# Kernel tuning notes

Hardware: AMD Instinct MI355X
Metric: run time of the kernel (lower is better)

## Reference

```python
import jax, jax.numpy as jnp
import numpy as np

G = 128          # graphs in batch
NPG = 2048       # nodes per graph (all graphs equal-sized; >= K so no topk padding)
N = G * NPG      # total nodes
MUT_PER_G = 2    # mutation CA atoms per graph
M = G * MUT_PER_G  # total centers (fixed for jit)
CA_ID = 1
K = 64           # module init k
BIG = jnp.float32(1e30)


def setup_inputs() -> dict:
    key = jax.random.key(0)
    k1, k2 = jax.random.split(key)
    node_position = jax.random.normal(k1, (N, 3), dtype=jnp.float32) * 10.0
    node2graph = jnp.repeat(jnp.arange(G, dtype=jnp.int32), NPG)
    local_idx = jnp.arange(N, dtype=jnp.int32) % NPG
    is_mutation = local_idx < MUT_PER_G                     # 2 mutation sites per graph
    atom_name = jax.random.randint(k2, (N,), 0, 38, dtype=jnp.int32)
    atom_name = jnp.where(is_mutation, CA_ID, atom_name)    # mutation sites are CA atoms
    num_nodes = jnp.full((G,), NPG, dtype=jnp.int32)
    return {"node_position": node_position, "is_mutation": is_mutation,
            "atom_name": atom_name, "node2graph": node2graph,
            "num_nodes": num_nodes, "ca_id": CA_ID}


def reference(node_position, is_mutation, atom_name, node2graph, num_nodes, ca_id):
    Gn = num_nodes.shape[0]
    Nn = node_position.shape[0]
    # mutation_mask = is_mutation & (atom_name == CA)
    mutation_mask = is_mutation & (atom_name == ca_id)
    # gather centers with fixed size M (jit-compatible ragged -> padded)
    center_idx = jnp.nonzero(mutation_mask, size=M, fill_value=0)[0]
    center_valid = jnp.arange(M) < mutation_mask.sum()
    cpos = node_position[center_idx]              # [M, 3]
    mut2graph = node2graph[center_idx]            # [M]
    x2 = jnp.sum(node_position * node_position, -1)           # [N]
    c2 = jnp.sum(cpos * cpos, -1)                             # [M]
    cross = node_position @ cpos.T                            # [N, M]
    d2 = x2[:, None] + c2[None, :] - 2.0 * cross
    ok = (node2graph[:, None] == mut2graph[None, :]) & center_valid[None, :]
    center_indices = jnp.argmin(jnp.where(ok, d2, BIG), axis=1)  # [N]
    # exact squared distance to assigned center (recomputed as in original)
    diff = node_position - cpos[center_indices]
    dist = jnp.sum(diff * diff, -1)
    dist = jnp.where(mutation_mask, 0.0, dist)
    # variadic_topk(dist, num_nodes, K, largest=False): pad per-graph rows with BIG
    start = jnp.cumsum(num_nodes) - num_nodes                  # [G]
    local = jnp.arange(Nn, dtype=jnp.int32) - start[node2graph]
    padded = jnp.full((Gn, NPG), BIG, dtype=dist.dtype).at[node2graph, local].set(dist)
    _, cols = jax.lax.top_k(-padded, K)                        # smallest-K per graph
    selected = (start[:, None] + cols).reshape(-1)             # global node indices
    node_mask = jnp.zeros((Nn,), dtype=bool).at[selected].set(True)
    return node_mask
```

## Files before the change

kernel.cpp:

```cpp
#include <hip/hip_runtime.h>

#define TPB     1024
#define NPGMAX  2048
#define EPT     (NPGMAX / TPB)
#define NW      (TPB / 64)
#define KSEL    64
#define WCAP    8
#define NGRP    8
#define HROW    260
#define BIGF    1e30f

__device__ __forceinline__ int mut_val(const unsigned* __restrict__ mu, int gi, int mode) {
    if (mode == 0) return (int)mu[gi];
    if (mode == 1) return (int)((mu[gi >> 2] >> ((gi & 3) * 8)) & 0xFFu);
    return __uint_as_float(mu[gi]) != 0.0f ? 1 : 0;
}

__device__ __forceinline__ int swz(int b) { return ((b & 7) << 5) | (b >> 3); }

extern "C" __global__ void __launch_bounds__(TPB)
knn_mask_kernel(const float* __restrict__ pos,
                const unsigned* __restrict__ mu,
                const int* __restrict__ atom,
                const int* __restrict__ num_nodes,
                const int* __restrict__ ca_ptr,
                int* __restrict__ out)
{
    const int g    = blockIdx.x;
    const int tid  = threadIdx.x;
    const int lane = tid & 63;
    const int wv   = tid >> 6;

    __shared__ int      s_hist[NGRP][HROW];
    __shared__ unsigned s_ck[NPGMAX];
    __shared__ int      s_cl[NPGMAX];
    __shared__ float    s_cwx[NW*WCAP], s_cwy[NW*WCAP], s_cwz[NW*WCAP], s_cw2[NW*WCAP];
    __shared__ int      s_wcnt[NW];
    __shared__ int      s_ccnt;
    __shared__ int      s_sel[2];
    __shared__ unsigned s_resT;
    __shared__ int      s_resL;

    const int ca = ca_ptr[0];
    const unsigned w0 = mu[0];
    const int mode = (w0 == 1u) ? 0 : (w0 == 257u) ? 1 : 2;

    {
        int* hp = &s_hist[0][0];
        for (int i = tid; i < NGRP * HROW; i += TPB) hp[i] = 0;
    }
    if (tid == 0) s_ccnt = 0;

    int part = 0;
    for (int i = lane; i < g; i += 64) part += num_nodes[i];
    for (int o = 32; o > 0; o >>= 1) part += __shfl_xor(part, o, 64);
    const int start = part;
    const int num   = num_nodes[g];

    float px[EPT], py[EPT], pz[EPT];
    bool  mreg[EPT];
    int wbase = 0;
    #pragma unroll
    for (int j = 0; j < EPT; ++j) {
        int li = tid + j * TPB;
        float x = 0.f, y = 0.f, z = 0.f;
        bool m = false;
        if (li < num) {
            int gi = start + li;
            x = pos[3 * gi]; y = pos[3 * gi + 1]; z = pos[3 * gi + 2];
            m = mut_val(mu, gi, mode) && (atom[gi] == ca);
        }
        px[j] = x; py[j] = y; pz[j] = z; mreg[j] = m;
        unsigned long long mm = __ballot(m);
        if (m) {
            int slot = wbase + __popcll(mm & ((1ull << lane) - 1ull));
            if (slot < WCAP) {
                int idx = wv * WCAP + slot;
                s_cwx[idx] = x; s_cwy[idx] = y; s_cwz[idx] = z;
                s_cw2[idx] = x * x + y * y + z * z;
            }
        }
        wbase += __popcll(mm);
    }
    if (lane == 0) s_wcnt[wv] = (wbase > WCAP) ? WCAP : wbase;
    __syncthreads();

    const int grp = wv & (NGRP - 1);
    unsigned kreg[EPT];
    #pragma unroll
    for (int j = 0; j < EPT; ++j) {
        float x = px[j], y = py[j], z = pz[j];
        float x2 = x * x + y * y + z * z;
        float bestd2 = BIGF, bx = 0.f, by = 0.f, bz = 0.f;
        bool found = false;
        for (int w = 0; w < NW; ++w) {
            int c0 = s_wcnt[w];
            for (int c = 0; c < c0; ++c) {
                int idx = w * WCAP + c;
                float cx = s_cwx[idx], cy = s_cwy[idx], cz = s_cwz[idx];
                float d2 = x2 + s_cw2[idx] - 2.0f * (x * cx + y * cy + z * cz);
                if (d2 < bestd2) { bestd2 = d2; bx = cx; by = cy; bz = cz; found = true; }
            }
        }
        float d = BIGF;
        int li = tid + j * TPB;
        if (li < num && found) {
            float dx = x - bx, dy = y - by, dz = z - bz;
            d = dx * dx + dy * dy + dz * dz;
            if (mreg[j]) d = 0.0f;
        }
        unsigned k = __float_as_uint(d);
        kreg[j] = k;
        atomicAdd(&s_hist[grp][swz((int)(k >> 23))], 1);
    }
    __syncthreads();

    if (wv == 0) {
        int h[4], tot = 0;
        #pragma unroll
        for (int b = 0; b < 4; ++b) {
            int sb = swz(lane * 4 + b), v = 0;
            #pragma unroll
            for (int q = 0; q < NGRP; ++q) v += s_hist[q][sb];
            h[b] = v; tot += v;
        }
        int incl = tot;
        for (int o = 1; o < 64; o <<= 1) { int v = __shfl_up(incl, o, 64); if (lane >= o) incl += v; }
        int run = incl - tot;
        int dig = -1, rem = 0;
        #pragma unroll
        for (int b = 0; b < 4; ++b) {
            if (run < KSEL && KSEL <= run + h[b]) { dig = lane * 4 + b; rem = KSEL - run; }
            run += h[b];
        }
        unsigned long long f = __ballot(dig >= 0);
        int srcl = (int)__builtin_ctzll(f);
        dig = __shfl(dig, srcl, 64);
        rem = __shfl(rem, srcl, 64);
        if (lane == 0) { s_sel[0] = dig; s_sel[1] = rem; }
    }
    __syncthreads();

    const unsigned dig1 = (unsigned)s_sel[0];
    #pragma unroll
    for (int j = 0; j < EPT; ++j) {
        bool m = (kreg[j] >> 23) == dig1;
        unsigned long long mm = __ballot(m);
        int cnt = __popcll(mm);
        int base = 0;
        if (lane == 0 && cnt) base = atomicAdd(&s_ccnt, cnt);
        base = __shfl(base, 0, 64);
        if (m) {
            int p = base + __popcll(mm & ((1ull << lane) - 1ull));
            s_ck[p] = kreg[j];
            s_cl[p] = tid + j * TPB;
        }
    }
    __syncthreads();

    if (wv == 0) {
        int kn = s_sel[1];
        const int C = s_ccnt;
        int* h2 = &s_hist[0][0];
        unsigned T = dig1 << 23;
        const int shifts[3] = {15, 7, 0};
        const unsigned fmask[3] = {255u, 255u, 127u};
        for (int r = 0; r < 3; ++r) {
            const int sh = shifts[r];
            #pragma unroll
            for (int b = 0; b < 4; ++b) h2[lane * 4 + b] = 0;
            asm volatile("s_waitcnt lgkmcnt(0)" ::: "memory");
            __builtin_amdgcn_sched_barrier(0);
            for (int i = lane; i < C; i += 64) {
                unsigned k = s_ck[i];
                if ((k >> (sh + 8)) == (T >> (sh + 8)))
                    atomicAdd(&h2[swz((int)((k >> sh) & fmask[r]))], 1);
            }
            asm volatile("s_waitcnt lgkmcnt(0)" ::: "memory");
            __builtin_amdgcn_sched_barrier(0);
            int h[4], tot = 0;
            #pragma unroll
            for (int b = 0; b < 4; ++b) { h[b] = h2[swz(lane * 4 + b)]; tot += h[b]; }
            int incl = tot;
            for (int o = 1; o < 64; o <<= 1) { int v = __shfl_up(incl, o, 64); if (lane >= o) incl += v; }
            int run = incl - tot;
            int dig = -1, rem = 0;
            #pragma unroll
            for (int b = 0; b < 4; ++b) {
                if (run < kn && kn <= run + h[b]) { dig = lane * 4 + b; rem = kn - run; }
                run += h[b];
            }
            unsigned long long f = __ballot(dig >= 0);
            int srcl = (int)__builtin_ctzll(f);
            dig = __shfl(dig, srcl, 64);
            rem = __shfl(rem, srcl, 64);
            T |= ((unsigned)dig) << sh;
            kn = rem;
        }
        int cut = -1;
        for (int it = 0; it < kn; ++it) {
            int mn = 0x7FFFFFFF;
            for (int i = lane; i < C; i += 64)
                if (s_ck[i] == T && s_cl[i] > cut) mn = min(mn, s_cl[i]);
            for (int o = 32; o > 0; o >>= 1) mn = min(mn, __shfl_xor(mn, o, 64));
            cut = mn;
        }
        if (lane == 0) { s_resT = T; s_resL = cut; }
    }
    __syncthreads();

    const unsigned T   = s_resT;
    const int      cut = s_resL;
    #pragma unroll
    for (int j = 0; j < EPT; ++j) {
        int li = tid + j * TPB;
        unsigned k = kreg[j];
        int sel = (k < T || (k == T && li <= cut)) ? 1 : 0;
        if (li < num) out[start + li] = sel;
    }
}

extern "C" void kernel_launch(void* const* d_in, const int* in_sizes, int n_in,
                              void* d_out, int out_size, void* d_ws, size_t ws_size,
                              hipStream_t stream) {
    const float*    pos       = (const float*)d_in[0];
    const unsigned* mu        = (const unsigned*)d_in[1];
    const int*      atom      = (const int*)d_in[2];
    const int*      num_nodes = (const int*)d_in[4];
    const int*      ca_ptr    = (const int*)d_in[5];
    int*            out       = (int*)d_out;

    const int g = in_sizes[4];
    knn_mask_kernel<<<g, TPB, 0, stream>>>(pos, mu, atom, num_nodes, ca_ptr, out);
}
```

Baseline: 13.31 us.

## Use 12-bit first radix pass and wave-level rank select for small candidate sets

The first radix-select pass now builds a single 4096-bin histogram on the top 12 bits of the key instead of replicated 256-bin histograms. The crossing bin is found with a two-level wave scan. When the candidate bucket holds at most 64 keys, the threshold is found by an all-pairs rank within one wavefront, which skips the remaining three histogram passes and the serial tie-break loop. Center collection moves to one global shared atomic counter instead of per-wave ballot slots. In exchange there are more histogram bins to zero and scan, more possible atomic contention on hot bins, and a larger LDS footprint.

```diff
diff --git a/kernel.cpp b/kernel.cpp
--- a/kernel.cpp
+++ b/kernel.cpp
@@ -5,9 +5,8 @@
 #define EPT     (NPGMAX / TPB)
 #define NW      (TPB / 64)
 #define KSEL    64
-#define WCAP    8
-#define NGRP    8
-#define HROW    260
+#define MAXC    64
+#define NBIN    4096
 #define BIGF    1e30f
 
 __device__ __forceinline__ int mut_val(const unsigned* __restrict__ mu, int gi, int mode) {
@@ -16,7 +15,8 @@
     return __uint_as_float(mu[gi]) != 0.0f ? 1 : 0;
 }
 
-__device__ __forceinline__ int swz(int b) { return ((b & 7) << 5) | (b >> 3); }
+__device__ __forceinline__ int swz12(int b) { return b ^ ((b >> 6) & 31); }
+__device__ __forceinline__ int swz8(int b) { return ((b & 7) << 5) | (b >> 3); }
 
 extern "C" __global__ void __launch_bounds__(TPB)
 knn_mask_kernel(const float* __restrict__ pos,
@@ -31,11 +31,11 @@
     const int lane = tid & 63;
     const int wv   = tid >> 6;
 
-    __shared__ int      s_hist[NGRP][HROW];
+    __shared__ int      s_hist[NBIN];
     __shared__ unsigned s_ck[NPGMAX];
     __shared__ int      s_cl[NPGMAX];
-    __shared__ float    s_cwx[NW*WCAP], s_cwy[NW*WCAP], s_cwz[NW*WCAP], s_cw2[NW*WCAP];
-    __shared__ int      s_wcnt[NW];
+    __shared__ float    s_cx[MAXC], s_cy[MAXC], s_cz[MAXC], s_c2[MAXC];
+    __shared__ int      s_cnt;
     __shared__ int      s_ccnt;
     __shared__ int      s_sel[2];
     __shared__ unsigned s_resT;
@@ -45,11 +45,9 @@
     const unsigned w0 = mu[0];
     const int mode = (w0 == 1u) ? 0 : (w0 == 257u) ? 1 : 2;
 
-    {
-        int* hp = &s_hist[0][0];
-        for (int i = tid; i < NGRP * HROW; i += TPB) hp[i] = 0;
-    }
-    if (tid == 0) s_ccnt = 0;
+    #pragma unroll
+    for (int i = 0; i < NBIN / TPB; ++i) s_hist[tid + i * TPB] = 0;
+    if (tid == 0) { s_cnt = 0; s_ccnt = 0; }
 
     int part = 0;
     for (int i = lane; i < g; i += 64) part += num_nodes[i];
@@ -59,7 +57,6 @@
 
     float px[EPT], py[EPT], pz[EPT];
     bool  mreg[EPT];
-    int wbase = 0;
     #pragma unroll
     for (int j = 0; j < EPT; ++j) {
         int li = tid + j * TPB;
@@ -71,21 +68,18 @@
             m = mut_val(mu, gi, mode) && (atom[gi] == ca);
         }
         px[j] = x; py[j] = y; pz[j] = z; mreg[j] = m;
-        unsigned long long mm = __ballot(m);
         if (m) {
-            int slot = wbase + __popcll(mm & ((1ull << lane) - 1ull));
-            if (slot < WCAP) {
-                int idx = wv * WCAP + slot;
-                s_cwx[idx] = x; s_cwy[idx] = y; s_cwz[idx] = z;
-                s_cw2[idx] = x * x + y * y + z * z;
-            }
-        }
-        wbase += __popcll(mm);
-    }
-    if (lane == 0) s_wcnt[wv] = (wbase > WCAP) ? WCAP : wbase;
-    __syncthreads();
-
-    const int grp = wv & (NGRP - 1);
+            int slot = atomicAdd(&s_cnt, 1);
+            if (slot < MAXC) {
+                s_cx[slot] = x; s_cy[slot] = y; s_cz[slot] = z;
+                s_c2[slot] = x * x + y * y + z * z;
+            }
+        }
+    }
+    __syncthreads();
+    const int craw = s_cnt;
+    const int cnt  = (craw > MAXC) ? MAXC : craw;
+
     unsigned kreg[EPT];
     #pragma unroll
     for (int j = 0; j < EPT; ++j) {
@@ -93,14 +87,10 @@
         float x2 = x * x + y * y + z * z;
         float bestd2 = BIGF, bx = 0.f, by = 0.f, bz = 0.f;
         bool found = false;
-        for (int w = 0; w < NW; ++w) {
-            int c0 = s_wcnt[w];
-            for (int c = 0; c < c0; ++c) {
-                int idx = w * WCAP + c;
-                float cx = s_cwx[idx], cy = s_cwy[idx], cz = s_cwz[idx];
-                float d2 = x2 + s_cw2[idx] - 2.0f * (x * cx + y * cy + z * cz);
-                if (d2 < bestd2) { bestd2 = d2; bx = cx; by = cy; bz = cz; found = true; }
-            }
+        for (int c = 0; c < cnt; ++c) {
+            float cx = s_cx[c], cy = s_cy[c], cz = s_cz[c];
+            float d2 = x2 + s_c2[c] - 2.0f * (x * cx + y * cy + z * cz);
+            if (d2 < bestd2) { bestd2 = d2; bx = cx; by = cy; bz = cz; found = true; }
         }
         float d = BIGF;
         int li = tid + j * TPB;
@@ -111,44 +101,44 @@
         }
         unsigned k = __float_as_uint(d);
         kreg[j] = k;
-        atomicAdd(&s_hist[grp][swz((int)(k >> 23))], 1);
+        atomicAdd(&s_hist[swz12((int)(k >> 19))], 1);
     }
     __syncthreads();
 
     if (wv == 0) {
-        int h[4], tot = 0;
-        #pragma unroll
-        for (int b = 0; b < 4; ++b) {
-            int sb = swz(lane * 4 + b), v = 0;
-            #pragma unroll
-            for (int q = 0; q < NGRP; ++q) v += s_hist[q][sb];
-            h[b] = v; tot += v;
-        }
+        int tot = 0;
+        for (int i = 0; i < 64; ++i) tot += s_hist[(lane << 6) + (i ^ (lane & 31))];
         int incl = tot;
         for (int o = 1; o < 64; o <<= 1) { int v = __shfl_up(incl, o, 64); if (lane >= o) incl += v; }
-        int run = incl - tot;
-        int dig = -1, rem = 0;
-        #pragma unroll
-        for (int b = 0; b < 4; ++b) {
-            if (run < KSEL && KSEL <= run + h[b]) { dig = lane * 4 + b; rem = KSEL - run; }
-            run += h[b];
-        }
-        unsigned long long f = __ballot(dig >= 0);
-        int srcl = (int)__builtin_ctzll(f);
-        dig = __shfl(dig, srcl, 64);
-        rem = __shfl(rem, srcl, 64);
-        if (lane == 0) { s_sel[0] = dig; s_sel[1] = rem; }
+        int excl = incl - tot;
+        bool cross = (excl < KSEL) && (KSEL <= incl);
+        unsigned long long cb = __ballot(cross);
+        int cl_  = (int)__builtin_ctzll(cb);
+        int base = __shfl(excl, cl_, 64);
+        int h1 = s_hist[(cl_ << 6) + (lane ^ (cl_ & 31))];
+        int incl2 = h1;
+        for (int o = 1; o < 64; o <<= 1) { int v = __shfl_up(incl2, o, 64); if (lane >= o) incl2 += v; }
+        int excl2 = incl2 - h1;
+        int kn1 = KSEL - base;
+        bool cross2 = (excl2 < kn1) && (kn1 <= incl2);
+        unsigned long long cb2 = __ballot(cross2);
+        int bl = (int)__builtin_ctzll(cb2);
+        int kv = __shfl(excl2, bl, 64);
+        if (lane == 0) {
+            s_sel[0] = (cl_ << 6) + bl;
+            s_sel[1] = kn1 - kv;
+        }
     }
     __syncthreads();
 
     const unsigned dig1 = (unsigned)s_sel[0];
     #pragma unroll
     for (int j = 0; j < EPT; ++j) {
-        bool m = (kreg[j] >> 23) == dig1;
+        bool m = (kreg[j] >> 19) == dig1;
         unsigned long long mm = __ballot(m);
-        int cnt = __popcll(mm);
+        int c_ = __popcll(mm);
         int base = 0;
-        if (lane == 0 && cnt) base = atomicAdd(&s_ccnt, cnt);
+        if (lane == 0 && c_) base = atomicAdd(&s_ccnt, c_);
         base = __shfl(base, 0, 64);
         if (m) {
             int p = base + __popcll(mm & ((1ull << lane) - 1ull));
@@ -159,53 +149,70 @@
     __syncthreads();
 
     if (wv == 0) {
+        const int C  = s_ccnt;
         int kn = s_sel[1];
-        const int C = s_ccnt;
-        int* h2 = &s_hist[0][0];
-        unsigned T = dig1 << 23;
-        const int shifts[3] = {15, 7, 0};
-        const unsigned fmask[3] = {255u, 255u, 127u};
-        for (int r = 0; r < 3; ++r) {
-            const int sh = shifts[r];
-            #pragma unroll
-            for (int b = 0; b < 4; ++b) h2[lane * 4 + b] = 0;
-            asm volatile("s_waitcnt lgkmcnt(0)" ::: "memory");
-            __builtin_amdgcn_sched_barrier(0);
-            for (int i = lane; i < C; i += 64) {
-                unsigned k = s_ck[i];
-                if ((k >> (sh + 8)) == (T >> (sh + 8)))
-                    atomicAdd(&h2[swz((int)((k >> sh) & fmask[r]))], 1);
-            }
-            asm volatile("s_waitcnt lgkmcnt(0)" ::: "memory");
-            __builtin_amdgcn_sched_barrier(0);
-            int h[4], tot = 0;
-            #pragma unroll
-            for (int b = 0; b < 4; ++b) { h[b] = h2[swz(lane * 4 + b)]; tot += h[b]; }
-            int incl = tot;
-            for (int o = 1; o < 64; o <<= 1) { int v = __shfl_up(incl, o, 64); if (lane >= o) incl += v; }
-            int run = incl - tot;
-            int dig = -1, rem = 0;
-            #pragma unroll
-            for (int b = 0; b < 4; ++b) {
-                if (run < kn && kn <= run + h[b]) { dig = lane * 4 + b; rem = kn - run; }
-                run += h[b];
-            }
-            unsigned long long f = __ballot(dig >= 0);
-            int srcl = (int)__builtin_ctzll(f);
-            dig = __shfl(dig, srcl, 64);
-            rem = __shfl(rem, srcl, 64);
-            T |= ((unsigned)dig) << sh;
-            kn = rem;
-        }
-        int cut = -1;
-        for (int it = 0; it < kn; ++it) {
-            int mn = 0x7FFFFFFF;
-            for (int i = lane; i < C; i += 64)
-                if (s_ck[i] == T && s_cl[i] > cut) mn = min(mn, s_cl[i]);
-            for (int o = 32; o > 0; o >>= 1) mn = min(mn, __shfl_xor(mn, o, 64));
-            cut = mn;
-        }
-        if (lane == 0) { s_resT = T; s_resL = cut; }
+        if (C <= 64) {
+            unsigned k = 0xFFFFFFFFu; int l = 0x7FFFFFFF;
+            if (lane < C) { k = s_ck[lane]; l = s_cl[lane]; }
+            int rank = 0;
+            for (int s = 1; s < 64; ++s) {
+                unsigned ko = __shfl_xor(k, s, 64);
+                int      lo = __shfl_xor(l, s, 64);
+                if (ko < k || (ko == k && lo < l)) ++rank;
+            }
+            bool hit = (lane < C) && (rank == kn - 1);
+            unsigned long long hb = __ballot(hit);
+            int hl = (int)__builtin_ctzll(hb);
+            unsigned Ts = __shfl(k, hl, 64);
+            int      Ls = __shfl(l, hl, 64);
+            if (lane == 0) { s_resT = Ts; s_resL = Ls; }
+        } else {
+            int* h2 = &s_hist[0];
+            unsigned T = dig1 << 19;
+            const int shifts[3] = {11, 3, 0};
+            const unsigned fmask[3] = {255u, 255u, 7u};
+            for (int r = 0; r < 3; ++r) {
+                const int sh = shifts[r];
+                #pragma unroll
+                for (int b = 0; b < 4; ++b) h2[lane * 4 + b] = 0;
+                asm volatile("s_waitcnt lgkmcnt(0)" ::: "memory");
+                __builtin_amdgcn_sched_barrier(0);
+                for (int i = lane; i < C; i += 64) {
+                    unsigned k = s_ck[i];
+                    if ((k >> (sh + 8)) == (T >> (sh + 8)))
+                        atomicAdd(&h2[swz8((int)((k >> sh) & fmask[r]))], 1);
+                }
+                asm volatile("s_waitcnt lgkmcnt(0)" ::: "memory");
+                __builtin_amdgcn_sched_barrier(0);
+                int h[4], tot = 0;
+                #pragma unroll
+                for (int b = 0; b < 4; ++b) { h[b] = h2[swz8(lane * 4 + b)]; tot += h[b]; }
+                int incl = tot;
+                for (int o = 1; o < 64; o <<= 1) { int v = __shfl_up(incl, o, 64); if (lane >= o) incl += v; }
+                int run = incl - tot;
+                int dig = -1, rem = 0;
+                #pragma unroll
+                for (int b = 0; b < 4; ++b) {
+                    if (run < kn && kn <= run + h[b]) { dig = lane * 4 + b; rem = kn - run; }
+                    run += h[b];
+                }
+                unsigned long long f = __ballot(dig >= 0);
+                int srcl = (int)__builtin_ctzll(f);
+                dig = __shfl(dig, srcl, 64);
+                rem = __shfl(rem, srcl, 64);
+                T |= ((unsigned)dig) << sh;
+                kn = rem;
+            }
+            int cut = -1;
+            for (int it = 0; it < kn; ++it) {
+                int mn = 0x7FFFFFFF;
+                for (int i = lane; i < C; i += 64)
+                    if (s_ck[i] == T && s_cl[i] > cut) mn = min(mn, s_cl[i]);
+                for (int o = 32; o > 0; o >>= 1) mn = min(mn, __shfl_xor(mn, o, 64));
+                cut = mn;
+            }
+            if (lane == 0) { s_resT = T; s_resL = cut; }
+        }
     }
     __syncthreads();
 
```

Result: slower. 16.10 us (+21.0%).
